# Kernel optimization log

Measured on AMD Instinct MI355X. Metric: run time of the kernel, lower is better.

The kernel has to match this reference:

```python
import jax, jax.numpy as jnp
import numpy as np
import math
from math import factorial
from fractions import Fraction

LMAX = 2
N_ATOMS = 30000
N_FEAT = 128


def _cg(j1, m1, j2, m2, j3, m3):
    # Clebsch-Gordan coefficient <j1 m1 j2 m2 | j3 m3> (Racah formula, exact rationals)
    if m3 != m1 + m2 or j3 < abs(j1 - j2) or j3 > j1 + j2:
        return 0.0
    f = factorial
    pref = Fraction((2 * j3 + 1) * f(j3 + j1 - j2) * f(j3 - j1 + j2) * f(j1 + j2 - j3), f(j1 + j2 + j3 + 1))
    pref *= f(j3 + m3) * f(j3 - m3) * f(j1 - m1) * f(j1 + m1) * f(j2 - m2) * f(j2 + m2)
    s = Fraction(0)
    kmin = max(0, j2 - j3 - m1, j1 - j3 + m2)
    kmax = min(j1 + j2 - j3, j1 - m1, j2 + m2)
    for k in range(kmin, kmax + 1):
        s += Fraction((-1) ** k, f(k) * f(j1 + j2 - j3 - k) * f(j1 - m1 - k) * f(j2 + m2 - k) * f(j3 - j2 + m1 + k) * f(j3 - j1 - m2 + k))
    return math.sqrt(float(pref)) * float(s)


def _sh_indices(lmax):
    lidx = np.concatenate([np.full(2 * l + 1, l) for l in range(lmax + 1)])
    midx = np.concatenate([np.arange(-l, l + 1) for l in range(lmax + 1)])
    return lidx, midx


def _build_sparse_cg(lmax):
    # dense complex-SH CG tensor over combined (l,m) index s, size S=(lmax+1)^2
    lidx, midx = _sh_indices(lmax)
    S = len(lidx)
    cg = np.zeros((S, S, S))
    for a in range(S):
        for b in range(S):
            for c in range(S):
                cg[a, b, c] = _cg(int(lidx[a]), int(midx[a]), int(lidx[b]), int(midx[b]), int(lidx[c]), int(midx[c]))
    # unitary complex SH -> real SH transform (rows: real, cols: complex)
    m1 = midx[:, None]
    m2 = midx[None, :]
    U = ((m1 == 0) & (m2 == 0)) * (1.0 + 0.0j)
    U = U + ((m1 > 0) & (m2 > 0) & (m1 == m2)) * ((-1.0) ** m1 / math.sqrt(2))
    U = U + ((m1 > 0) & (m2 < 0) & (m1 == -m2)) * (1.0 / math.sqrt(2))
    U = U + ((m1 < 0) & (m2 > 0) & (m1 == -m2)) * (-1.0j * (-1.0) ** m1 / math.sqrt(2))
    U = U + ((m1 < 0) & (m2 < 0) & (m1 == m2)) * (1.0j / math.sqrt(2))
    U = U * (lidx[:, None] == lidx[None, :])
    cg_rsh = np.einsum('ijk,mi,nj,ok->mno', cg.astype(np.complex128), U, U, U.conj())
    # parity invariance mask
    parity = (-1.0) ** lidx
    pmask = (parity[:, None, None] * parity[None, :, None]) == parity[None, None, :]
    cg_real = (cg_rsh * pmask).real
    # sparsify (threshold kills complex-arithmetic residues ~1e-17)
    i1, i2, io = np.nonzero(np.abs(cg_real) > 1e-12)
    return cg_real[i1, i2, io].astype(np.float32), i1.astype(np.int32), i2.astype(np.int32), io.astype(np.int32)


def setup_inputs() -> dict:
    key = jax.random.key(0)
    k1, k2 = jax.random.split(key)
    S = (LMAX + 1) ** 2
    cg_sparse, i1, i2, io = _build_sparse_cg(LMAX)
    return {
        'x1': jax.random.normal(k1, (N_ATOMS, S, N_FEAT), dtype=jnp.float32),
        'x2': jax.random.normal(k2, (N_ATOMS, S, N_FEAT), dtype=jnp.float32),
        'cg_sparse': jnp.asarray(cg_sparse),
        'idx_in_1': jnp.asarray(i1),
        'idx_in_2': jnp.asarray(i2),
        'idx_out': jnp.asarray(io),
    }


def reference(x1, x2, cg_sparse, idx_in_1, idx_in_2, idx_out):
    S = (LMAX + 1) ** 2
    # gather paths [n_atoms, P, F], multiply by sparse CG, scatter-add over output (l,m)
    y = x1[:, idx_in_1, :] * x2[:, idx_in_2, :] * cg_sparse[None, :, None]
    out = jnp.zeros((x1.shape[0], S, x1.shape[2]), x1.dtype).at[:, idx_out, :].add(y)
    return out
```

## Files before the change

### kernel.cpp

```cpp
#include <hip/hip_runtime.h>


#define NS 9
#define NF 128
#define NF4 32

typedef float vf4 __attribute__((ext_vector_type(4)));

constexpr int LQ[9] = {0, 1, 1, 1, 2, 2, 2, 2, 2};
constexpr int MQ[9] = {0, -1, 0, 1, -2, -1, 0, 1, 2};

constexpr bool cg_compat(int A, int B, int O) {
  const int l1 = LQ[A], l2 = LQ[B], l3 = LQ[O];
  const int m1 = MQ[A], m2 = MQ[B], m3 = MQ[O];
  const int lo = (l1 > l2) ? (l1 - l2) : (l2 - l1);
  if (l3 < lo || l3 > l1 + l2) return false;
  if ((l1 + l2 + l3) & 1) return false;
  const int u = (m1 < 0) ? -m1 : m1;
  const int v = (m2 < 0) ? -m2 : m2;
  const int w = (m3 < 0) ? -m3 : m3;
  const int d = (u > v) ? (u - v) : (v - u);
  if (!(w == u + v || w == d)) return false;
  const bool mixed = (m1 < 0) != (m2 < 0);
  if (mixed != (m3 < 0)) return false;
  return true;
}

__global__ void build_dense_cg(const float* __restrict__ cg,
                               const int* __restrict__ i1,
                               const int* __restrict__ i2,
                               const int* __restrict__ io,
                               int nnz, float* __restrict__ C) {
  const int t = threadIdx.x;
  for (int i = t; i < NS * NS * NS; i += blockDim.x) C[i] = 0.0f;
  __syncthreads();
  for (int k = t; k < nnz; k += blockDim.x) {
    C[io[k] * (NS * NS) + i1[k] * NS + i2[k]] = cg[k];
  }
}

__global__ __launch_bounds__(256, 4) void so3_tp_kernel(
    const float4* __restrict__ x1, const float4* __restrict__ x2,
    const float* __restrict__ C, float4* __restrict__ out, int total) {
  const int tid = blockIdx.x * 256 + threadIdx.x;
  if (tid >= total) return;
  const int atom = tid >> 5;
  const int f4 = tid & 31;
  const int base = atom * (NS * NF4) + f4;

  const float4* ap = x1 + base;
  const float4* bp = x2 + base;

  float4 a[NS], b[NS];
#pragma unroll
  for (int s = 0; s < NS; s++) a[s] = ap[s * NF4];
#pragma unroll
  for (int s = 0; s < NS; s++) b[s] = bp[s * NF4];

  float4* op = out + base;
#pragma unroll
  for (int o = 0; o < NS; o++) {
    float4 acc = make_float4(0.f, 0.f, 0.f, 0.f);
#pragma unroll
    for (int ia = 0; ia < NS; ia++) {
#pragma unroll
      for (int ib = 0; ib < NS; ib++) {
        if (cg_compat(ia, ib, o)) {
          const float c = C[o * (NS * NS) + ia * NS + ib];
          acc.x = fmaf(c, a[ia].x * b[ib].x, acc.x);
          acc.y = fmaf(c, a[ia].y * b[ib].y, acc.y);
          acc.z = fmaf(c, a[ia].z * b[ib].z, acc.z);
          acc.w = fmaf(c, a[ia].w * b[ib].w, acc.w);
        }
      }
    }
    __builtin_nontemporal_store(*(const vf4*)&acc, (vf4*)(op + o * NF4));
  }
}

extern "C" void kernel_launch(void* const* d_in, const int* in_sizes, int n_in,
                              void* d_out, int out_size, void* d_ws, size_t ws_size,
                              hipStream_t stream) {
  const float* x1 = (const float*)d_in[0];
  const float* x2 = (const float*)d_in[1];
  const float* cg = (const float*)d_in[2];
  const int* i1 = (const int*)d_in[3];
  const int* i2 = (const int*)d_in[4];
  const int* io = (const int*)d_in[5];

  const int nnz = in_sizes[2];
  const int natoms = in_sizes[0] / (NS * NF);
  float* C = (float*)d_ws;

  build_dense_cg<<<1, 256, 0, stream>>>(cg, i1, i2, io, nnz, C);

  const int total = natoms * NF4;
  const int blocks = (total + 255) / 256;
  so3_tp_kernel<<<blocks, 256, 0, stream>>>((const float4*)x1, (const float4*)x2, C,
                                            (float4*)d_out, total);
}
```

Baseline: 341.4 us.

## Use persistent grid-stride kernel with register double-buffered prefetch of inputs

Replaces the one-thread-per-element launch with a grid capped at 960 blocks that loops over elements with a grid stride. Each thread prefetches the next element's 18 float4 inputs into a second register buffer while computing the current one, so load latency overlaps compute. It also lowers launch_bounds occupancy from 4 to 2 blocks to make room for the extra registers, and swaps the nontemporal stores for plain stores. The risk is fewer resident waves to hide latency on a kernel that is bound by memory bandwidth, plus possible register spills.

```diff
diff --git a/kernel.cpp b/kernel.cpp
--- a/kernel.cpp
+++ b/kernel.cpp
@@ -4,8 +4,6 @@
 #define NS 9
 #define NF 128
 #define NF4 32
-
-typedef float vf4 __attribute__((ext_vector_type(4)));
 
 constexpr int LQ[9] = {0, 1, 1, 1, 2, 2, 2, 2, 2};
 constexpr int MQ[9] = {0, -1, 0, 1, -2, -1, 0, 1, 2};
@@ -39,25 +37,24 @@
   }
 }
 
-__global__ __launch_bounds__(256, 4) void so3_tp_kernel(
-    const float4* __restrict__ x1, const float4* __restrict__ x2,
-    const float* __restrict__ C, float4* __restrict__ out, int total) {
-  const int tid = blockIdx.x * 256 + threadIdx.x;
-  if (tid >= total) return;
-  const int atom = tid >> 5;
-  const int f4 = tid & 31;
+__device__ __forceinline__ void load18(const float4* __restrict__ x1,
+                                       const float4* __restrict__ x2,
+                                       int idx, float4* a, float4* b) {
+  const int atom = idx >> 5;
+  const int f4 = idx & 31;
   const int base = atom * (NS * NF4) + f4;
+#pragma unroll
+  for (int s = 0; s < NS; s++) a[s] = x1[base + s * NF4];
+#pragma unroll
+  for (int s = 0; s < NS; s++) b[s] = x2[base + s * NF4];
+}
 
-  const float4* ap = x1 + base;
-  const float4* bp = x2 + base;
-
-  float4 a[NS], b[NS];
-#pragma unroll
-  for (int s = 0; s < NS; s++) a[s] = ap[s * NF4];
-#pragma unroll
-  for (int s = 0; s < NS; s++) b[s] = bp[s * NF4];
-
-  float4* op = out + base;
+__device__ __forceinline__ void compute_store(const float* __restrict__ C,
+                                              const float4* a, const float4* b,
+                                              float4* __restrict__ out, int idx) {
+  const int atom = idx >> 5;
+  const int f4 = idx & 31;
+  const int base = atom * (NS * NF4) + f4;
 #pragma unroll
   for (int o = 0; o < NS; o++) {
     float4 acc = make_float4(0.f, 0.f, 0.f, 0.f);
@@ -74,7 +71,33 @@
         }
       }
     }
-    __builtin_nontemporal_store(*(const vf4*)&acc, (vf4*)(op + o * NF4));
+    out[base + o * NF4] = acc;
+  }
+}
+
+__global__ __launch_bounds__(256, 2) void so3_tp_kernel(
+    const float4* __restrict__ x1, const float4* __restrict__ x2,
+    const float* __restrict__ C, float4* __restrict__ out, int total) {
+  int idx = blockIdx.x * 256 + threadIdx.x;
+  const int stride = gridDim.x * 256;
+
+  float4 A1[NS], B1[NS], A2[NS], B2[NS];
+
+  if (idx >= total) return;
+  load18(x1, x2, idx, A1, B1);
+
+  while (true) {
+    int n1 = idx + stride;
+    if (n1 < total) load18(x1, x2, n1, A2, B2);
+    compute_store(C, A1, B1, out, idx);
+    if (n1 >= total) return;
+    idx = n1;
+
+    int n2 = idx + stride;
+    if (n2 < total) load18(x1, x2, n2, A1, B1);
+    compute_store(C, A2, B2, out, idx);
+    if (n2 >= total) return;
+    idx = n2;
   }
 }
 
@@ -95,7 +118,8 @@
   build_dense_cg<<<1, 256, 0, stream>>>(cg, i1, i2, io, nnz, C);
 
   const int total = natoms * NF4;
-  const int blocks = (total + 255) / 256;
+  int blocks = (total + 255) / 256;
+  if (blocks > 960) blocks = 960;
   so3_tp_kernel<<<blocks, 256, 0, stream>>>((const float4*)x1, (const float4*)x2, C,
                                             (float4*)d_out, total);
 }
```

Result: faster. 334.2 us (-2.1%).
